# Optimization experiments

Hardware: AMD Instinct MI355X
Metric: run time of the kernel (lower is better)

## Reference

```python
import jax, jax.numpy as jnp
import numpy as np
import math

DIM = 32
M_CONST = 10000.0
TIME_SCALE = 30000.0 / 500.0 * 0.3  # 18.0


def sinusoidal_emb(x):
    # x: [...] -> [..., DIM]
    half = DIM // 2
    freqs = jnp.exp(jnp.arange(half, dtype=x.dtype) * (-math.log(M_CONST) / half))
    ang = x[..., None] * freqs  # [..., half]
    return jnp.concatenate([jnp.sin(ang), jnp.cos(ang)], axis=-1)


def setup_inputs() -> dict:
    key = jax.random.key(0)
    k1, k2, k3, k4 = jax.random.split(key, 4)
    B, N = 2, 1024
    pos = jax.random.normal(k1, (B, N, 3), dtype=jnp.float32)
    time = jax.random.normal(k2, (B, N), dtype=jnp.float32)
    # nn.Linear(32, 32) params
    lim = 1.0 / math.sqrt(DIM)
    W = jax.random.uniform(k3, (DIM, DIM), minval=-lim, maxval=lim, dtype=jnp.float32)
    b = jax.random.uniform(k4, (DIM,), minval=-lim, maxval=lim, dtype=jnp.float32)
    return {"pos": pos, "time": time, "W": W, "b": b}


def reference(pos, time, W, b):
    # pairwise squared spatial distance minus scaled squared time difference
    dpos = pos[:, :, None, :] - pos[:, None, :, :]          # [B,N,N,3]
    dt = (time[:, :, None] - time[:, None, :]) * TIME_SCALE  # [B,N,N]
    ds2 = jnp.sum(dpos * dpos, axis=-1) - dt * dt            # [B,N,N]
    a = jnp.abs(ds2)
    d = jnp.sign(ds2) * jnp.sqrt(a)
    emb = sinusoidal_emb(1024.0 * jnp.clip(d, -4.0, 4.0))    # [B,N,N,DIM]
    rel_attn = jnp.einsum('bnmd,ed->bnme', emb, W) + b       # Linear(dim,dim)
    return (rel_attn, emb)
```

## Files before the change

kernel.cpp:

```cpp
#include <hip/hip_runtime.h>
#include <hip/hip_bf16.h>

typedef __bf16 bf16x8 __attribute__((ext_vector_type(8)));
typedef float  f32x4  __attribute__((ext_vector_type(4)));

__constant__ __device__ const float FREQ8[8] = {
    1.0f, 0.5623413251903491f, 0.31622776601683794f, 0.17782794100389228f,
    0.1f, 0.05623413251903491f, 0.031622776601683794f, 0.017782794100389228f };

template<bool POW2>
__global__ __launch_bounds__(256, 5) void relds_mfma(
    const float* __restrict__ pos,
    const float* __restrict__ tim,
    const float* __restrict__ W,
    const float* __restrict__ bias,
    float* __restrict__ out_attn,
    float* __restrict__ out_emb,
    int N, int NN, int P, int logN)
{
    const int tid  = threadIdx.x;
    const int lane = tid & 63;
    const int wave = tid >> 6;
    const int row  = lane & 15;
    const int kb   = lane >> 4;

    bf16x8 Wf[2];
    f32x4  bq[2];
    #pragma unroll
    for (int n = 0; n < 2; ++n) {
        const int e = n * 16 + row;
        const float4 wA = *reinterpret_cast<const float4*>(W + e * 32 + kb * 8);
        const float4 wB = *reinterpret_cast<const float4*>(W + e * 32 + kb * 8 + 4);
        Wf[n][0] = (__bf16)wA.x; Wf[n][1] = (__bf16)wA.y;
        Wf[n][2] = (__bf16)wA.z; Wf[n][3] = (__bf16)wA.w;
        Wf[n][4] = (__bf16)wB.x; Wf[n][5] = (__bf16)wB.y;
        Wf[n][6] = (__bf16)wB.z; Wf[n][7] = (__bf16)wB.w;
        const float4 bb = *reinterpret_cast<const float4*>(bias + n * 16 + kb * 4);
        bq[n][0] = bb.x; bq[n][1] = bb.y; bq[n][2] = bb.z; bq[n][3] = bb.w;
    }

    const int wbase = blockIdx.x * 256 + wave * 64;
    if (wbase >= P) return;

    constexpr float INV2PI = 0.15915494309189535f;
    const float premul = INV2PI * ((kb & 1) ? 0.01f : 1.0f);
    const float qoff   = (kb >= 2) ? 0.25f : 0.0f;

    #pragma unroll
    for (int t = 0; t < 4; ++t) {
        const int q  = wbase + t * 16 + row;
        const int qc = (q < P) ? q : (P - 1);
        int in_n, in_m;
        if (POW2) {
            in_n = qc >> logN;
            in_m = ((qc >> (2 * logN)) << logN) | (qc & (N - 1));
        } else {
            const int b_ = qc / NN; const int r_ = qc - b_ * NN;
            const int n_ = r_ / N;  const int m_ = r_ - n_ * N;
            in_n = b_ * N + n_;     in_m = b_ * N + m_;
        }
        const float dx = pos[in_n * 3 + 0] - pos[in_m * 3 + 0];
        const float dy = pos[in_n * 3 + 1] - pos[in_m * 3 + 1];
        const float dz = pos[in_n * 3 + 2] - pos[in_m * 3 + 2];
        const float dt = (tim[in_n] - tim[in_m]) * 18.0f;
        const float ds2 = dx * dx + dy * dy + dz * dz - dt * dt;
        const float d   = copysignf(sqrtf(fabsf(ds2)), ds2);
        const float x   = 1024.0f * fminf(4.0f, fmaxf(-4.0f, d));
        const float xr  = x * premul;

        float v[8];
        #pragma unroll
        for (int j = 0; j < 8; ++j) {
            float rr = fmaf(xr, FREQ8[j], qoff);
            rr -= floorf(rr);
            v[j] = __builtin_amdgcn_sinf(rr);
        }

        if (q < P) {
            float* ep = out_emb + (size_t)q * 32 + kb * 8;
            f32x4 e0 = { v[0], v[1], v[2], v[3] };
            f32x4 e1 = { v[4], v[5], v[6], v[7] };
            reinterpret_cast<f32x4*>(ep)[0] = e0;
            reinterpret_cast<f32x4*>(ep)[1] = e1;
        }

        bf16x8 Af;
        #pragma unroll
        for (int j = 0; j < 8; ++j) Af[j] = (__bf16)v[j];
        f32x4 acc0 = __builtin_amdgcn_mfma_f32_16x16x32_bf16(Wf[0], Af, bq[0], 0, 0, 0);
        f32x4 acc1 = __builtin_amdgcn_mfma_f32_16x16x32_bf16(Wf[1], Af, bq[1], 0, 0, 0);

        if (q < P) {
            float* ap = out_attn + (size_t)q * 32 + kb * 4;
            *reinterpret_cast<f32x4*>(ap)      = acc0;
            *reinterpret_cast<f32x4*>(ap + 16) = acc1;
        }
    }
}

extern "C" void kernel_launch(void* const* d_in, const int* in_sizes, int n_in,
                              void* d_out, int out_size, void* d_ws, size_t ws_size,
                              hipStream_t stream) {
    const float* pos  = (const float*)d_in[0];
    const float* tim  = (const float*)d_in[1];
    const float* W    = (const float*)d_in[2];
    const float* bias = (const float*)d_in[3];

    const int BN = in_sizes[1];
    const int P  = out_size / 64;
    const int N  = P / BN;
    const int NN = N * N;

    int logN = 0;
    while ((1 << logN) < N) ++logN;
    const bool pow2 = ((1 << logN) == N);

    float* out_attn = (float*)d_out;
    float* out_emb  = out_attn + (size_t)out_size / 2;

    const int grid = (P + 255) / 256;
    if (pow2)
        relds_mfma<true><<<grid, 256, 0, stream>>>(pos, tim, W, bias, out_attn, out_emb, N, NN, P, logN);
    else
        relds_mfma<false><<<grid, 256, 0, stream>>>(pos, tim, W, bias, out_attn, out_emb, N, NN, P, logN);
}
```

Measured before the change: 107.6 us.

## Use persistent blocks with double-buffered input prefetch across chunks

```diff
diff --git a/kernel.cpp b/kernel.cpp
--- a/kernel.cpp
+++ b/kernel.cpp
@@ -9,20 +9,24 @@
     0.1f, 0.05623413251903491f, 0.031622776601683794f, 0.017782794100389228f };
 
 template<bool POW2>
-__global__ __launch_bounds__(256, 5) void relds_mfma(
+__global__ __launch_bounds__(256, 4) void relds_mfma(
     const float* __restrict__ pos,
     const float* __restrict__ tim,
     const float* __restrict__ W,
     const float* __restrict__ bias,
     float* __restrict__ out_attn,
     float* __restrict__ out_emb,
-    int N, int NN, int P, int logN)
+    int N, int NN, int P, int logN, int nchunks, int cpb)
 {
     const int tid  = threadIdx.x;
     const int lane = tid & 63;
     const int wave = tid >> 6;
     const int row  = lane & 15;
     const int kb   = lane >> 4;
+
+    const int c0 = blockIdx.x * cpb;
+    if (c0 >= nchunks) return;
+    const int c1 = (c0 + cpb < nchunks) ? (c0 + cpb) : nchunks;
 
     bf16x8 Wf[2];
     f32x4  bq[2];
@@ -39,63 +43,81 @@
         bq[n][0] = bb.x; bq[n][1] = bb.y; bq[n][2] = bb.z; bq[n][3] = bb.w;
     }
 
-    const int wbase = blockIdx.x * 256 + wave * 64;
-    if (wbase >= P) return;
-
     constexpr float INV2PI = 0.15915494309189535f;
     const float premul = INV2PI * ((kb & 1) ? 0.01f : 1.0f);
     const float qoff   = (kb >= 2) ? 0.25f : 0.0f;
 
-    #pragma unroll
-    for (int t = 0; t < 4; ++t) {
-        const int q  = wbase + t * 16 + row;
-        const int qc = (q < P) ? q : (P - 1);
-        int in_n, in_m;
-        if (POW2) {
-            in_n = qc >> logN;
-            in_m = ((qc >> (2 * logN)) << logN) | (qc & (N - 1));
-        } else {
-            const int b_ = qc / NN; const int r_ = qc - b_ * NN;
-            const int n_ = r_ / N;  const int m_ = r_ - n_ * N;
-            in_n = b_ * N + n_;     in_m = b_ * N + m_;
-        }
-        const float dx = pos[in_n * 3 + 0] - pos[in_m * 3 + 0];
-        const float dy = pos[in_n * 3 + 1] - pos[in_m * 3 + 1];
-        const float dz = pos[in_n * 3 + 2] - pos[in_m * 3 + 2];
-        const float dt = (tim[in_n] - tim[in_m]) * 18.0f;
-        const float ds2 = dx * dx + dy * dy + dz * dz - dt * dt;
-        const float d   = copysignf(sqrtf(fabsf(ds2)), ds2);
-        const float x   = 1024.0f * fminf(4.0f, fmaxf(-4.0f, d));
-        const float xr  = x * premul;
+    float A[4][8], Bb[4][8];
 
-        float v[8];
-        #pragma unroll
-        for (int j = 0; j < 8; ++j) {
-            float rr = fmaf(xr, FREQ8[j], qoff);
-            rr -= floorf(rr);
-            v[j] = __builtin_amdgcn_sinf(rr);
-        }
+#define LOADC(chunk, buf) { \
+    const int _qb = (chunk) * 256 + wave * 64 + row; \
+    _Pragma("unroll") \
+    for (int t = 0; t < 4; ++t) { \
+        const int q  = _qb + t * 16; \
+        const int qc = (q < P) ? q : (P - 1); \
+        int in_n, in_m; \
+        if (POW2) { \
+            in_n = qc >> logN; \
+            in_m = ((qc >> (2 * logN)) << logN) | (qc & (N - 1)); \
+        } else { \
+            const int b_ = qc / NN; const int r_ = qc - b_ * NN; \
+            const int n_ = r_ / N;  const int m_ = r_ - n_ * N; \
+            in_n = b_ * N + n_;     in_m = b_ * N + m_; \
+        } \
+        buf[t][0] = pos[in_n * 3 + 0]; buf[t][1] = pos[in_n * 3 + 1]; \
+        buf[t][2] = pos[in_n * 3 + 2]; buf[t][3] = pos[in_m * 3 + 0]; \
+        buf[t][4] = pos[in_m * 3 + 1]; buf[t][5] = pos[in_m * 3 + 2]; \
+        buf[t][6] = tim[in_n];         buf[t][7] = tim[in_m]; \
+    } }
 
-        if (q < P) {
-            float* ep = out_emb + (size_t)q * 32 + kb * 8;
-            f32x4 e0 = { v[0], v[1], v[2], v[3] };
-            f32x4 e1 = { v[4], v[5], v[6], v[7] };
-            reinterpret_cast<f32x4*>(ep)[0] = e0;
-            reinterpret_cast<f32x4*>(ep)[1] = e1;
-        }
+#define PROCC(chunk, buf) { \
+    const int _qb = (chunk) * 256 + wave * 64 + row; \
+    _Pragma("unroll") \
+    for (int t = 0; t < 4; ++t) { \
+        const int q = _qb + t * 16; \
+        const float dx = buf[t][0] - buf[t][3]; \
+        const float dy = buf[t][1] - buf[t][4]; \
+        const float dz = buf[t][2] - buf[t][5]; \
+        const float dt = (buf[t][6] - buf[t][7]) * 18.0f; \
+        const float ds2 = dx * dx + dy * dy + dz * dz - dt * dt; \
+        const float d   = copysignf(sqrtf(fabsf(ds2)), ds2); \
+        const float x   = 1024.0f * fminf(4.0f, fmaxf(-4.0f, d)); \
+        const float xr  = x * premul; \
+        float v[8]; \
+        _Pragma("unroll") \
+        for (int j = 0; j < 8; ++j) { \
+            float rr = fmaf(xr, FREQ8[j], qoff); \
+            rr -= floorf(rr); \
+            v[j] = __builtin_amdgcn_sinf(rr); \
+        } \
+        if (q < P) { \
+            float* ep = out_emb + (size_t)q * 32 + kb * 8; \
+            f32x4 e0 = { v[0], v[1], v[2], v[3] }; \
+            f32x4 e1 = { v[4], v[5], v[6], v[7] }; \
+            reinterpret_cast<f32x4*>(ep)[0] = e0; \
+            reinterpret_cast<f32x4*>(ep)[1] = e1; \
+        } \
+        bf16x8 Af; \
+        _Pragma("unroll") \
+        for (int j = 0; j < 8; ++j) Af[j] = (__bf16)v[j]; \
+        f32x4 a0 = __builtin_amdgcn_mfma_f32_16x16x32_bf16(Wf[0], Af, bq[0], 0, 0, 0); \
+        f32x4 a1 = __builtin_amdgcn_mfma_f32_16x16x32_bf16(Wf[1], Af, bq[1], 0, 0, 0); \
+        if (q < P) { \
+            float* ap = out_attn + (size_t)q * 32 + kb * 4; \
+            *reinterpret_cast<f32x4*>(ap)      = a0; \
+            *reinterpret_cast<f32x4*>(ap + 16) = a1; \
+        } \
+    } }
 
-        bf16x8 Af;
-        #pragma unroll
-        for (int j = 0; j < 8; ++j) Af[j] = (__bf16)v[j];
-        f32x4 acc0 = __builtin_amdgcn_mfma_f32_16x16x32_bf16(Wf[0], Af, bq[0], 0, 0, 0);
-        f32x4 acc1 = __builtin_amdgcn_mfma_f32_16x16x32_bf16(Wf[1], Af, bq[1], 0, 0, 0);
-
-        if (q < P) {
-            float* ap = out_attn + (size_t)q * 32 + kb * 4;
-            *reinterpret_cast<f32x4*>(ap)      = acc0;
-            *reinterpret_cast<f32x4*>(ap + 16) = acc1;
-        }
+    LOADC(c0, A)
+    for (int c = c0; c < c1; c += 2) {
+        if (c + 1 < c1) LOADC(c + 1, Bb)
+        PROCC(c, A)
+        if (c + 2 < c1) LOADC(c + 2, A)
+        if (c + 1 < c1) PROCC(c + 1, Bb)
     }
+#undef LOADC
+#undef PROCC
 }
 
 extern "C" void kernel_launch(void* const* d_in, const int* in_sizes, int n_in,
@@ -118,9 +140,12 @@
     float* out_attn = (float*)d_out;
     float* out_emb  = out_attn + (size_t)out_size / 2;
 
-    const int grid = (P + 255) / 256;
+    const int nchunks = (P + 255) / 256;
+    const int grid    = 1024;
+    const int cpb     = (nchunks + grid - 1) / grid;
+
     if (pow2)
-        relds_mfma<true><<<grid, 256, 0, stream>>>(pos, tim, W, bias, out_attn, out_emb, N, NN, P, logN);
+        relds_mfma<true><<<grid, 256, 0, stream>>>(pos, tim, W, bias, out_attn, out_emb, N, NN, P, logN, nchunks, cpb);
     else
-        relds_mfma<false><<<grid, 256, 0, stream>>>(pos, tim, W, bias, out_attn, out_emb, N, NN, P, logN);
+        relds_mfma<false><<<grid, 256, 0, stream>>>(pos, tim, W, bias, out_attn, out_emb, N, NN, P, logN, nchunks, cpb);
 }
```

Measured after the change: 109.9 us. 1.02x slower.

## Split emb and attn outputs into separate interleaved blocks, recomputing embedding

Applied to the files above, without the earlier changes.

```diff
diff --git a/kernel.cpp b/kernel.cpp
--- a/kernel.cpp
+++ b/kernel.cpp
@@ -9,7 +9,7 @@
     0.1f, 0.05623413251903491f, 0.031622776601683794f, 0.017782794100389228f };
 
 template<bool POW2>
-__global__ __launch_bounds__(256, 5) void relds_mfma(
+__global__ __launch_bounds__(256, 5) void relds_split(
     const float* __restrict__ pos,
     const float* __restrict__ tim,
     const float* __restrict__ W,
@@ -24,76 +24,107 @@
     const int row  = lane & 15;
     const int kb   = lane >> 4;
 
-    bf16x8 Wf[2];
-    f32x4  bq[2];
-    #pragma unroll
-    for (int n = 0; n < 2; ++n) {
-        const int e = n * 16 + row;
-        const float4 wA = *reinterpret_cast<const float4*>(W + e * 32 + kb * 8);
-        const float4 wB = *reinterpret_cast<const float4*>(W + e * 32 + kb * 8 + 4);
-        Wf[n][0] = (__bf16)wA.x; Wf[n][1] = (__bf16)wA.y;
-        Wf[n][2] = (__bf16)wA.z; Wf[n][3] = (__bf16)wA.w;
-        Wf[n][4] = (__bf16)wB.x; Wf[n][5] = (__bf16)wB.y;
-        Wf[n][6] = (__bf16)wB.z; Wf[n][7] = (__bf16)wB.w;
-        const float4 bb = *reinterpret_cast<const float4*>(bias + n * 16 + kb * 4);
-        bq[n][0] = bb.x; bq[n][1] = bb.y; bq[n][2] = bb.z; bq[n][3] = bb.w;
-    }
-
-    const int wbase = blockIdx.x * 256 + wave * 64;
+    const int side = blockIdx.x & 1;
+    const int pid  = blockIdx.x >> 1;
+    const int wbase = pid * 256 + wave * 64;
     if (wbase >= P) return;
 
     constexpr float INV2PI = 0.15915494309189535f;
     const float premul = INV2PI * ((kb & 1) ? 0.01f : 1.0f);
     const float qoff   = (kb >= 2) ? 0.25f : 0.0f;
 
-    #pragma unroll
-    for (int t = 0; t < 4; ++t) {
-        const int q  = wbase + t * 16 + row;
-        const int qc = (q < P) ? q : (P - 1);
-        int in_n, in_m;
-        if (POW2) {
-            in_n = qc >> logN;
-            in_m = ((qc >> (2 * logN)) << logN) | (qc & (N - 1));
-        } else {
-            const int b_ = qc / NN; const int r_ = qc - b_ * NN;
-            const int n_ = r_ / N;  const int m_ = r_ - n_ * N;
-            in_n = b_ * N + n_;     in_m = b_ * N + m_;
-        }
-        const float dx = pos[in_n * 3 + 0] - pos[in_m * 3 + 0];
-        const float dy = pos[in_n * 3 + 1] - pos[in_m * 3 + 1];
-        const float dz = pos[in_n * 3 + 2] - pos[in_m * 3 + 2];
-        const float dt = (tim[in_n] - tim[in_m]) * 18.0f;
-        const float ds2 = dx * dx + dy * dy + dz * dz - dt * dt;
-        const float d   = copysignf(sqrtf(fabsf(ds2)), ds2);
-        const float x   = 1024.0f * fminf(4.0f, fmaxf(-4.0f, d));
-        const float xr  = x * premul;
-
-        float v[8];
+    if (side == 0) {
+        bf16x8 Wf[2];
+        f32x4  bq[2];
         #pragma unroll
-        for (int j = 0; j < 8; ++j) {
-            float rr = fmaf(xr, FREQ8[j], qoff);
-            rr -= floorf(rr);
-            v[j] = __builtin_amdgcn_sinf(rr);
+        for (int n = 0; n < 2; ++n) {
+            const int e = n * 16 + row;
+            const float4 wA = *reinterpret_cast<const float4*>(W + e * 32 + kb * 8);
+            const float4 wB = *reinterpret_cast<const float4*>(W + e * 32 + kb * 8 + 4);
+            Wf[n][0] = (__bf16)wA.x; Wf[n][1] = (__bf16)wA.y;
+            Wf[n][2] = (__bf16)wA.z; Wf[n][3] = (__bf16)wA.w;
+            Wf[n][4] = (__bf16)wB.x; Wf[n][5] = (__bf16)wB.y;
+            Wf[n][6] = (__bf16)wB.z; Wf[n][7] = (__bf16)wB.w;
+            const float4 bb = *reinterpret_cast<const float4*>(bias + n * 16 + kb * 4);
+            bq[n][0] = bb.x; bq[n][1] = bb.y; bq[n][2] = bb.z; bq[n][3] = bb.w;
         }
 
-        if (q < P) {
-            float* ep = out_emb + (size_t)q * 32 + kb * 8;
-            f32x4 e0 = { v[0], v[1], v[2], v[3] };
-            f32x4 e1 = { v[4], v[5], v[6], v[7] };
-            reinterpret_cast<f32x4*>(ep)[0] = e0;
-            reinterpret_cast<f32x4*>(ep)[1] = e1;
+        #pragma unroll
+        for (int t = 0; t < 4; ++t) {
+            const int q  = wbase + t * 16 + row;
+            const int qc = (q < P) ? q : (P - 1);
+            int in_n, in_m;
+            if (POW2) {
+                in_n = qc >> logN;
+                in_m = ((qc >> (2 * logN)) << logN) | (qc & (N - 1));
+            } else {
+                const int b_ = qc / NN; const int r_ = qc - b_ * NN;
+                const int n_ = r_ / N;  const int m_ = r_ - n_ * N;
+                in_n = b_ * N + n_;     in_m = b_ * N + m_;
+            }
+            const float dx = pos[in_n * 3 + 0] - pos[in_m * 3 + 0];
+            const float dy = pos[in_n * 3 + 1] - pos[in_m * 3 + 1];
+            const float dz = pos[in_n * 3 + 2] - pos[in_m * 3 + 2];
+            const float dt = (tim[in_n] - tim[in_m]) * 18.0f;
+            const float ds2 = dx * dx + dy * dy + dz * dz - dt * dt;
+            const float d   = copysignf(sqrtf(fabsf(ds2)), ds2);
+            const float x   = 1024.0f * fminf(4.0f, fmaxf(-4.0f, d));
+            const float xr  = x * premul;
+
+            bf16x8 Af;
+            #pragma unroll
+            for (int j = 0; j < 8; ++j) {
+                float rr = fmaf(xr, FREQ8[j], qoff);
+                rr -= floorf(rr);
+                Af[j] = (__bf16)__builtin_amdgcn_sinf(rr);
+            }
+            f32x4 acc0 = __builtin_amdgcn_mfma_f32_16x16x32_bf16(Wf[0], Af, bq[0], 0, 0, 0);
+            f32x4 acc1 = __builtin_amdgcn_mfma_f32_16x16x32_bf16(Wf[1], Af, bq[1], 0, 0, 0);
+
+            if (q < P) {
+                float* ap = out_attn + (size_t)q * 32 + kb * 4;
+                *reinterpret_cast<f32x4*>(ap)      = acc0;
+                *reinterpret_cast<f32x4*>(ap + 16) = acc1;
+            }
         }
+    } else {
+        #pragma unroll
+        for (int t = 0; t < 4; ++t) {
+            const int q  = wbase + t * 16 + row;
+            const int qc = (q < P) ? q : (P - 1);
+            int in_n, in_m;
+            if (POW2) {
+                in_n = qc >> logN;
+                in_m = ((qc >> (2 * logN)) << logN) | (qc & (N - 1));
+            } else {
+                const int b_ = qc / NN; const int r_ = qc - b_ * NN;
+                const int n_ = r_ / N;  const int m_ = r_ - n_ * N;
+                in_n = b_ * N + n_;     in_m = b_ * N + m_;
+            }
+            const float dx = pos[in_n * 3 + 0] - pos[in_m * 3 + 0];
+            const float dy = pos[in_n * 3 + 1] - pos[in_m * 3 + 1];
+            const float dz = pos[in_n * 3 + 2] - pos[in_m * 3 + 2];
+            const float dt = (tim[in_n] - tim[in_m]) * 18.0f;
+            const float ds2 = dx * dx + dy * dy + dz * dz - dt * dt;
+            const float d   = copysignf(sqrtf(fabsf(ds2)), ds2);
+            const float x   = 1024.0f * fminf(4.0f, fmaxf(-4.0f, d));
+            const float xr  = x * premul;
 
-        bf16x8 Af;
-        #pragma unroll
-        for (int j = 0; j < 8; ++j) Af[j] = (__bf16)v[j];
-        f32x4 acc0 = __builtin_amdgcn_mfma_f32_16x16x32_bf16(Wf[0], Af, bq[0], 0, 0, 0);
-        f32x4 acc1 = __builtin_amdgcn_mfma_f32_16x16x32_bf16(Wf[1], Af, bq[1], 0, 0, 0);
+            float v[8];
+            #pragma unroll
+            for (int j = 0; j < 8; ++j) {
+                float rr = fmaf(xr, FREQ8[j], qoff);
+                rr -= floorf(rr);
+                v[j] = __builtin_amdgcn_sinf(rr);
+            }
 
-        if (q < P) {
-            float* ap = out_attn + (size_t)q * 32 + kb * 4;
-            *reinterpret_cast<f32x4*>(ap)      = acc0;
-            *reinterpret_cast<f32x4*>(ap + 16) = acc1;
+            if (q < P) {
+                float* ep = out_emb + (size_t)q * 32 + kb * 8;
+                f32x4 e0 = { v[0], v[1], v[2], v[3] };
+                f32x4 e1 = { v[4], v[5], v[6], v[7] };
+                reinterpret_cast<f32x4*>(ep)[0] = e0;
+                reinterpret_cast<f32x4*>(ep)[1] = e1;
+            }
         }
     }
 }
@@ -118,9 +149,9 @@
     float* out_attn = (float*)d_out;
     float* out_emb  = out_attn + (size_t)out_size / 2;
 
-    const int grid = (P + 255) / 256;
+    const int grid = 2 * ((P + 255) / 256);
     if (pow2)
-        relds_mfma<true><<<grid, 256, 0, stream>>>(pos, tim, W, bias, out_attn, out_emb, N, NN, P, logN);
+        relds_split<true><<<grid, 256, 0, stream>>>(pos, tim, W, bias, out_attn, out_emb, N, NN, P, logN);
     else
-        relds_mfma<false><<<grid, 256, 0, stream>>>(pos, tim, W, bias, out_attn, out_emb, N, NN, P, logN);
+        relds_split<false><<<grid, 256, 0, stream>>>(pos, tim, W, bias, out_attn, out_emb, N, NN, P, logN);
 }
```

Measured after the change: 98.24 us. 1.1x faster.
